# Kernel tuning notes

Hardware: AMD Instinct MI355X
Metric: run time of the kernel (lower is better)

## Reference

```python
import jax, jax.numpy as jnp
import numpy as np

HIDDEN = 512


def setup_inputs() -> dict:
    key = jax.random.key(0)
    ks = jax.random.split(key, 5)
    S, B, I, H = 256, 128, 1024, HIDDEN
    scale_ih = 1.0 / np.sqrt(H)
    return {
        "x": jax.random.normal(ks[0], (S, B, I), dtype=jnp.float32),
        "w_ih": jax.random.normal(ks[1], (4 * H, I), dtype=jnp.float32) * scale_ih,
        "w_hh": jax.random.normal(ks[2], (4 * H, H), dtype=jnp.float32) * scale_ih,
        "b_ih": jax.random.normal(ks[3], (4 * H,), dtype=jnp.float32) * scale_ih,
        "b_hh": jax.random.normal(ks[4], (4 * H,), dtype=jnp.float32) * scale_ih,
    }


def reference(x, w_ih, w_hh, b_ih, b_hh):
    # x: [S, B, I]. LSTMCell with PyTorch gate order (i, f, g, o).
    S, B, _ = x.shape
    H = HIDDEN
    bias = b_ih + b_hh  # fuse both biases

    def step(carry, xt):
        h, c = carry
        gates = xt @ w_ih.T + h @ w_hh.T + bias  # [B, 4H]
        i, f, g, o = jnp.split(gates, 4, axis=-1)
        i = jax.nn.sigmoid(i)
        f = jax.nn.sigmoid(f)
        g = jnp.tanh(g)
        o = jax.nn.sigmoid(o)
        c = f * c + i * g
        h = o * jnp.tanh(c)
        # original code's h[arange(B)] / c[arange(B)] is an identity gather: no-op
        return (h, c), None

    h0 = jnp.zeros((B, H), dtype=x.dtype)
    c0 = jnp.zeros((B, H), dtype=x.dtype)
    (h, c), _ = jax.lax.scan(step, (h0, c0), x)
    return h.sum()
```

## Files before the change

kernel.cpp:

```cpp
#include <hip/hip_runtime.h>

typedef __attribute__((ext_vector_type(8))) short short8;
typedef __attribute__((ext_vector_type(4))) float f32x4;

#define S_LEN 256
#define BATCH 128
#define IN_DIM 1024
#define HID 512
#define G4 2048

#define SENT 0xFFFFFFFFu

#define LSTM_BLOCKS 128
#define GEMM_WORKERS 128
#define TOT_BLOCKS (LSTM_BLOCKS + GEMM_WORKERS)
#define NT_PER_ROW 8
#define N_TILES (256 * NT_PER_ROW)

__device__ unsigned g_cnt[S_LEN];

__device__ __forceinline__ unsigned short f32_bf16(float f) {
  unsigned int u = __float_as_uint(f);
  u = (u + 0x7FFFu + ((u >> 16) & 1u)) >> 16;
  return (unsigned short)u;
}
__device__ __forceinline__ float bf16_f32(unsigned short h) {
  return __uint_as_float(((unsigned int)h) << 16);
}
__device__ __forceinline__ float sigm(float x) { return 1.0f / (1.0f + __expf(-x)); }
__device__ __forceinline__ float tanh_fast(float x) {
  return 1.0f - 2.0f / (__expf(2.0f * x) + 1.0f);
}
__device__ __forceinline__ unsigned ld_cnt(const unsigned* p) {
  return __hip_atomic_load(p, __ATOMIC_RELAXED, __HIP_MEMORY_SCOPE_AGENT);
}
__device__ __forceinline__ unsigned ld_u32_agent(const void* p) {
  return __hip_atomic_load((const unsigned*)p, __ATOMIC_RELAXED, __HIP_MEMORY_SCOPE_AGENT);
}

__device__ __forceinline__ void cvt4(const float* __restrict__ s,
                                     unsigned short* __restrict__ d, int i) {
  float4 v = *(const float4*)(s + (size_t)i * 4);
  ushort4 o;
  o.x = f32_bf16(v.x); o.y = f32_bf16(v.y); o.z = f32_bf16(v.z); o.w = f32_bf16(v.w);
  *(ushort4*)(d + (size_t)i * 4) = o;
}

__global__ void prep(const float* __restrict__ x, const float* __restrict__ w_ih,
                     const float* __restrict__ w_hh, const float* __restrict__ b_ih,
                     const float* __restrict__ b_hh, unsigned short* __restrict__ x_bf,
                     unsigned short* __restrict__ wih_bf, unsigned short* __restrict__ whh_bf,
                     float* __restrict__ bias, uint4* __restrict__ hring4) {
  const int gtid = blockIdx.x * blockDim.x + threadIdx.x;
  const int gsz = gridDim.x * blockDim.x;
  if (gtid < G4) bias[gtid] = b_ih[gtid] + b_hh[gtid];
  if (gtid < S_LEN) g_cnt[gtid] = 0u;
  for (int i = gtid; i < 33554432 / 4; i += gsz) cvt4(x, x_bf, i);
  for (int i = gtid; i < 2097152 / 4; i += gsz) cvt4(w_ih, wih_bf, i);
  for (int i = gtid; i < 1048576 / 4; i += gsz) cvt4(w_hh, whh_bf, i);
  const int SLOT4 = BATCH * HID / 8;
  const int TOT4 = 257 * SLOT4;
  const uint4 z = make_uint4(0u, 0u, 0u, 0u);
  const uint4 sN = make_uint4(SENT, SENT, SENT, SENT);
  for (int k = gtid; k < TOT4; k += gsz) hring4[k] = (k < SLOT4) ? z : sN;
}

__device__ __forceinline__ void gl_lds16(const void* g, void* l) {
  __builtin_amdgcn_global_load_lds(
      (const __attribute__((address_space(1))) unsigned int*)g,
      (__attribute__((address_space(3))) unsigned int*)l, 16, 0, 0);
}

__global__ __launch_bounds__(512, 1) void fused_lstm(
    const unsigned short* __restrict__ whh,
    const unsigned short* __restrict__ xbf,
    const unsigned short* __restrict__ wih,
    const float* __restrict__ bias,
    unsigned short* __restrict__ gx,
    unsigned* __restrict__ hring,
    float* __restrict__ out) {
  __shared__ __align__(16) union {
    struct { unsigned short Hs[2][16][520]; float Gt[16][132]; } L;
    struct { unsigned short As[2 * 4096]; unsigned short Bs[2 * 8192]; } G;
  } sm;

  const int tid = threadIdx.x;
  const int w = tid >> 6, l = tid & 63;

  if (blockIdx.x >= LSTM_BLOCKS) {
    const int wm = w & 1, wn = w >> 1;
    for (int tile = (int)blockIdx.x - LSTM_BLOCKS; tile < N_TILES; tile += GEMM_WORKERS) {
      const int nt = tile & (NT_PER_ROW - 1), mt = tile >> 3;
      f32x4 acc[4][4];
#pragma unroll
      for (int i = 0; i < 4; i++)
#pragma unroll
        for (int j = 0; j < 4; j++) acc[i][j] = f32x4{0.f, 0.f, 0.f, 0.f};

      auto stage = [&](int cur, int k0) {
        {
          int row = tid >> 2, kc = tid & 3;
          gl_lds16(xbf + (size_t)(mt * 128 + row) * 1024 + k0 + kc * 8,
                   sm.G.As + cur * 4096 + w * 512);
        }
#pragma unroll
        for (int jj = 0; jj < 2; ++jj) {
          int cid = jj * 512 + tid;
          int row = cid >> 2, kc = cid & 3;
          gl_lds16(wih + (size_t)(nt * 256 + row) * 1024 + k0 + kc * 8,
                   sm.G.Bs + cur * 8192 + jj * 4096 + w * 512);
        }
      };

      stage(0, 0);
      asm volatile("s_waitcnt vmcnt(0)" ::: "memory");
      __builtin_amdgcn_s_barrier();

      for (int ks = 0; ks < 32; ++ks) {
        const int cur = ks & 1;
        if (ks + 1 < 32) stage(cur ^ 1, (ks + 1) * 32);
        short8 a[4], b[4];
#pragma unroll
        for (int i = 0; i < 4; i++)
          a[i] = *(const short8*)&sm.G.As[cur * 4096 +
                                          (wm * 64 + i * 16 + (l & 15)) * 32 + (l >> 4) * 8];
#pragma unroll
        for (int j = 0; j < 4; j++)
          b[j] = *(const short8*)&sm.G.Bs[cur * 8192 +
                                          (wn * 64 + j * 16 + (l & 15)) * 32 + (l >> 4) * 8];
#pragma unroll
        for (int i = 0; i < 4; i++)
#pragma unroll
          for (int j = 0; j < 4; j++)
            acc[i][j] = __builtin_amdgcn_mfma_f32_16x16x32_bf16(a[i], b[j], acc[i][j], 0, 0, 0);
        __builtin_amdgcn_sched_barrier(0);
        asm volatile("s_waitcnt vmcnt(0)" ::: "memory");
        __builtin_amdgcn_s_barrier();
      }

#pragma unroll
      for (int j = 0; j < 4; j++) {
        int cg = nt * 256 + wn * 64 + j * 16 + (l & 15);
        float bv = bias[cg];
#pragma unroll
        for (int i = 0; i < 4; i++) {
          int rbase = mt * 128 + wm * 64 + i * 16 + (l >> 4) * 4;
#pragma unroll
          for (int r = 0; r < 4; r++) {
            unsigned short hv = f32_bf16(acc[i][j][r] + bv);
            __hip_atomic_store(gx + (size_t)(rbase + r) * G4 + cg, hv,
                               __ATOMIC_RELAXED, __HIP_MEMORY_SCOPE_AGENT);
          }
        }
      }
      asm volatile("s_waitcnt vmcnt(0)" ::: "memory");
      __syncthreads();
      if (tid == 0)
        __hip_atomic_fetch_add(&g_cnt[mt], 1u, __ATOMIC_RELAXED, __HIP_MEMORY_SCOPE_AGENT);
    }
    return;
  }

  __builtin_amdgcn_s_setprio(1);
  if (tid >= 256) {
    for (int t = 0; t < S_LEN; t++) __syncthreads();
    return;
  }
  const int m = blockIdx.x & 7;
  const int s = blockIdx.x >> 3;

  short8 bw[16][2];
#pragma unroll
  for (int u = 0; u < 2; u++) {
    int n = (2 * w + u) * 16 + (l & 15);
    int jn = n >> 2, g = n & 3;
    int R = g * 512 + s * 32 + jn;
    const unsigned short* base = whh + (size_t)R * 512 + ((l >> 4) * 8);
#pragma unroll
    for (int kk = 0; kk < 16; kk++) bw[kk][u] = *(const short8*)(base + kk * 32);
  }

  const int b = l & 15;
  const int p = 4 * w + (l >> 4);
  const int gb = m * 16 + b;
  const int colg = s * 32 + 2 * p;
  float c0 = 0.f, c1 = 0.f;
  unsigned hp_last = 0u;

  const int SLOTW = BATCH * HID / 2;
  const unsigned long long* hull = (const unsigned long long*)hring;
  const int SLOTQ = BATCH * HID / 4;

  const int skc = tid & 127;
  const int srow = tid >> 7;
  const bool selfst = (((tid >> 3) & 15) == s);
  const size_t qbase = (size_t)(m * 16 + srow) * 128 + skc;

  unsigned long long v[8];
#pragma unroll
  for (int it = 0; it < 8; it++)
    v[it] = __hip_atomic_load(&hull[qbase + (size_t)it * 256],
                              __ATOMIC_RELAXED, __HIP_MEMORY_SCOPE_AGENT);
  while (ld_cnt(&g_cnt[0]) != (unsigned)NT_PER_ROW) __builtin_amdgcn_s_sleep(2);
  float2 pg[4];
  {
    size_t base0 = (size_t)gb * G4 + colg;
#pragma unroll
    for (int g = 0; g < 4; g++) {
      unsigned u = ld_u32_agent(gx + base0 + (size_t)g * 512);
      pg[g].x = bf16_f32((unsigned short)(u & 0xFFFFu));
      pg[g].y = bf16_f32((unsigned short)(u >> 16));
    }
  }
  unsigned cn = ld_cnt(&g_cnt[1]);

  for (int t = 0; t < S_LEN; t++) {
    const int buf = t & 1;
    const unsigned long long* src = hull + (size_t)t * SLOTQ;

    if (!(selfst && t > 0)) {
      for (;;) {
        int bad = 0;
#pragma unroll
        for (int it = 0; it < 8; it++)
          bad |= (((unsigned)v[it] == SENT) | ((unsigned)(v[it] >> 32) == SENT)) << it;
        if (!bad) break;
#pragma unroll
        for (int it = 0; it < 8; it++)
          if ((bad >> it) & 1)
            v[it] = __hip_atomic_load(&src[qbase + (size_t)it * 256],
                                      __ATOMIC_RELAXED, __HIP_MEMORY_SCOPE_AGENT);
      }
#pragma unroll
      for (int it = 0; it < 8; it++)
        *(unsigned long long*)&sm.L.Hs[buf][it * 2 + srow][skc * 4] = v[it];
    }
    __syncthreads();

    unsigned long long vn[8];
    float2 pgn[4];
    if (t + 1 < S_LEN) {
      if (!selfst) {
        const unsigned long long* srcn = hull + (size_t)(t + 1) * SLOTQ;
#pragma unroll
        for (int it = 0; it < 8; it++)
          vn[it] = __hip_atomic_load(&srcn[qbase + (size_t)it * 256],
                                     __ATOMIC_RELAXED, __HIP_MEMORY_SCOPE_AGENT);
      }
      if (cn != (unsigned)NT_PER_ROW) {
        do {
          __builtin_amdgcn_s_sleep(1);
          cn = ld_cnt(&g_cnt[t + 1]);
        } while (cn != (unsigned)NT_PER_ROW);
      }
      size_t basen = (size_t)((t + 1) * BATCH + gb) * G4 + colg;
#pragma unroll
      for (int g = 0; g < 4; g++) {
        unsigned u = ld_u32_agent(gx + basen + (size_t)g * 512);
        pgn[g].x = bf16_f32((unsigned short)(u & 0xFFFFu));
        pgn[g].y = bf16_f32((unsigned short)(u >> 16));
      }
      cn = (t + 2 < S_LEN) ? ld_cnt(&g_cnt[t + 2]) : (unsigned)NT_PER_ROW;
    }

    f32x4 acc0 = f32x4{0.f, 0.f, 0.f, 0.f};
    f32x4 acc1 = f32x4{0.f, 0.f, 0.f, 0.f};
#pragma unroll
    for (int kk = 0; kk < 16; kk++) {
      short8 a = *(const short8*)&sm.L.Hs[buf][l & 15][kk * 32 + (l >> 4) * 8];
      acc0 = __builtin_amdgcn_mfma_f32_16x16x32_bf16(a, bw[kk][0], acc0, 0, 0, 0);
      acc1 = __builtin_amdgcn_mfma_f32_16x16x32_bf16(a, bw[kk][1], acc1, 0, 0, 0);
    }

#pragma unroll
    for (int r = 0; r < 4; r++) {
      sm.L.Gt[(l >> 4) * 4 + r][(2 * w + 0) * 16 + (l & 15)] = acc0[r];
      sm.L.Gt[(l >> 4) * 4 + r][(2 * w + 1) * 16 + (l & 15)] = acc1[r];
    }

    float4 g0 = *(const float4*)&sm.L.Gt[b][8 * p];
    float4 g1 = *(const float4*)&sm.L.Gt[b][8 * p + 4];
    float i0 = sigm(g0.x + pg[0].x), f0 = sigm(g0.y + pg[1].x);
    float gg0 = tanh_fast(g0.z + pg[2].x), o0 = sigm(g0.w + pg[3].x);
    c0 = f0 * c0 + i0 * gg0;
    float h0 = o0 * tanh_fast(c0);
    float i1 = sigm(g1.x + pg[0].y), f1 = sigm(g1.y + pg[1].y);
    float gg1 = tanh_fast(g1.z + pg[2].y), o1 = sigm(g1.w + pg[3].y);
    c1 = f1 * c1 + i1 * gg1;
    float h1 = o1 * tanh_fast(c1);
    unsigned hp = (unsigned)f32_bf16(h0) | ((unsigned)f32_bf16(h1) << 16);
    hp_last = hp;

    __hip_atomic_store(&hring[(size_t)(t + 1) * SLOTW + gb * 256 + s * 16 + p], hp,
                       __ATOMIC_RELAXED, __HIP_MEMORY_SCOPE_AGENT);
    *(unsigned*)&sm.L.Hs[buf ^ 1][b][colg] = hp;

#pragma unroll
    for (int it = 0; it < 8; it++) v[it] = vn[it];
#pragma unroll
    for (int g = 0; g < 4; g++) pg[g] = pgn[g];
  }

  {
    float loc = bf16_f32((unsigned short)(hp_last & 0xFFFFu)) +
                bf16_f32((unsigned short)(hp_last >> 16));
#pragma unroll
    for (int off = 32; off > 0; off >>= 1) loc += __shfl_down(loc, off);
    if (l == 0) atomicAdd(out, loc);
  }
}

extern "C" void kernel_launch(void* const* d_in, const int* in_sizes, int n_in,
                              void* d_out, int out_size, void* d_ws, size_t ws_size,
                              hipStream_t stream) {
  const float* x = (const float*)d_in[0];
  const float* w_ih = (const float*)d_in[1];
  const float* w_hh = (const float*)d_in[2];
  const float* b_ih = (const float*)d_in[3];
  const float* b_hh = (const float*)d_in[4];

  char* ws = (char*)d_ws;
  unsigned short* x_bf = (unsigned short*)(ws);
  unsigned short* wih_bf = (unsigned short*)(ws + 67108864);
  unsigned short* whh_bf = (unsigned short*)(ws + 71303168);
  float* bias = (float*)(ws + 73400320);
  unsigned* hring = (unsigned*)(ws + 73408512);
  unsigned short* gx = (unsigned short*)(ws + 107094016);

  prep<<<2048, 256, 0, stream>>>(x, w_ih, w_hh, b_ih, b_hh, x_bf, wih_bf, whh_bf, bias,
                                 (uint4*)hring);

  fused_lstm<<<TOT_BLOCKS, 512, 0, stream>>>(whh_bf, x_bf, wih_bf, bias, gx, hring,
                                             (float*)d_out);
}
```

Before: 1.080 ms.

## Fuse x fp32-to-bf16 conversion into GEMM worker A-tile staging

Drops the separate prep pass that converted the whole 128 MB fp32 x tensor to bf16. GEMM workers now load fp32 x rows into registers, convert them to bf16 and write them to LDS, overlapped with the MFMA loop. This removes a full write and re-read of x_bf before the fused kernel starts. The cost is twice the global read bytes for A inside the GEMM and extra conversion ALU work. It also adds an asm register pin on the resident W_hh fragments to keep them in VGPRs, and halves the prep grid.

```diff
diff --git a/kernel.cpp b/kernel.cpp
--- a/kernel.cpp
+++ b/kernel.cpp
@@ -2,6 +2,7 @@
 
 typedef __attribute__((ext_vector_type(8))) short short8;
 typedef __attribute__((ext_vector_type(4))) float f32x4;
+typedef __attribute__((ext_vector_type(4))) int i32x4;
 
 #define S_LEN 256
 #define BATCH 128
@@ -36,6 +37,11 @@
 }
 __device__ __forceinline__ unsigned ld_u32_agent(const void* p) {
   return __hip_atomic_load((const unsigned*)p, __ATOMIC_RELAXED, __HIP_MEMORY_SCOPE_AGENT);
+}
+__device__ __forceinline__ short8 pin8(short8 x) {
+  i32x4 t = __builtin_bit_cast(i32x4, x);
+  asm volatile("" : "+v"(t));
+  return __builtin_bit_cast(short8, t);
 }
 
 __device__ __forceinline__ void cvt4(const float* __restrict__ s,
@@ -46,16 +52,14 @@
   *(ushort4*)(d + (size_t)i * 4) = o;
 }
 
-__global__ void prep(const float* __restrict__ x, const float* __restrict__ w_ih,
-                     const float* __restrict__ w_hh, const float* __restrict__ b_ih,
-                     const float* __restrict__ b_hh, unsigned short* __restrict__ x_bf,
+__global__ void prep(const float* __restrict__ w_ih, const float* __restrict__ w_hh,
+                     const float* __restrict__ b_ih, const float* __restrict__ b_hh,
                      unsigned short* __restrict__ wih_bf, unsigned short* __restrict__ whh_bf,
                      float* __restrict__ bias, uint4* __restrict__ hring4) {
   const int gtid = blockIdx.x * blockDim.x + threadIdx.x;
   const int gsz = gridDim.x * blockDim.x;
   if (gtid < G4) bias[gtid] = b_ih[gtid] + b_hh[gtid];
   if (gtid < S_LEN) g_cnt[gtid] = 0u;
-  for (int i = gtid; i < 33554432 / 4; i += gsz) cvt4(x, x_bf, i);
   for (int i = gtid; i < 2097152 / 4; i += gsz) cvt4(w_ih, wih_bf, i);
   for (int i = gtid; i < 1048576 / 4; i += gsz) cvt4(w_hh, whh_bf, i);
   const int SLOT4 = BATCH * HID / 8;
@@ -73,7 +77,7 @@
 
 __global__ __launch_bounds__(512, 1) void fused_lstm(
     const unsigned short* __restrict__ whh,
-    const unsigned short* __restrict__ xbf,
+    const float* __restrict__ x,
     const unsigned short* __restrict__ wih,
     const float* __restrict__ bias,
     unsigned short* __restrict__ gx,
@@ -89,6 +93,7 @@
 
   if (blockIdx.x >= LSTM_BLOCKS) {
     const int wm = w & 1, wn = w >> 1;
+    const int arow = tid >> 2, akc = tid & 3;
     for (int tile = (int)blockIdx.x - LSTM_BLOCKS; tile < N_TILES; tile += GEMM_WORKERS) {
       const int nt = tile & (NT_PER_ROW - 1), mt = tile >> 3;
       f32x4 acc[4][4];
@@ -97,12 +102,9 @@
 #pragma unroll
         for (int j = 0; j < 4; j++) acc[i][j] = f32x4{0.f, 0.f, 0.f, 0.f};
 
-      auto stage = [&](int cur, int k0) {
-        {
-          int row = tid >> 2, kc = tid & 3;
-          gl_lds16(xbf + (size_t)(mt * 128 + row) * 1024 + k0 + kc * 8,
-                   sm.G.As + cur * 4096 + w * 512);
-        }
+      const float* xrow = x + (size_t)(mt * 128 + arow) * 1024 + akc * 8;
+
+      auto issueB = [&](int cur, int k0) {
 #pragma unroll
         for (int jj = 0; jj < 2; ++jj) {
           int cid = jj * 512 + tid;
@@ -111,14 +113,32 @@
                    sm.G.Bs + cur * 8192 + jj * 4096 + w * 512);
         }
       };
-
-      stage(0, 0);
-      asm volatile("s_waitcnt vmcnt(0)" ::: "memory");
+      auto issueX = [&](int k0, float4& xa, float4& xb) {
+        xa = *(const float4*)(xrow + k0);
+        xb = *(const float4*)(xrow + k0 + 4);
+      };
+      auto commitX = [&](int cur, const float4& xa, const float4& xb) {
+        uint4 o;
+        o.x = (unsigned)f32_bf16(xa.x) | ((unsigned)f32_bf16(xa.y) << 16);
+        o.y = (unsigned)f32_bf16(xa.z) | ((unsigned)f32_bf16(xa.w) << 16);
+        o.z = (unsigned)f32_bf16(xb.x) | ((unsigned)f32_bf16(xb.y) << 16);
+        o.w = (unsigned)f32_bf16(xb.z) | ((unsigned)f32_bf16(xb.w) << 16);
+        *(uint4*)&sm.G.As[cur * 4096 + tid * 8] = o;
+      };
+
+      float4 xa, xb;
+      issueX(0, xa, xb);
+      issueB(0, 0);
+      commitX(0, xa, xb);
+      asm volatile("s_waitcnt vmcnt(0) lgkmcnt(0)" ::: "memory");
       __builtin_amdgcn_s_barrier();
 
       for (int ks = 0; ks < 32; ++ks) {
         const int cur = ks & 1;
-        if (ks + 1 < 32) stage(cur ^ 1, (ks + 1) * 32);
+        if (ks + 1 < 32) {
+          issueX((ks + 1) * 32, xa, xb);
+          issueB(cur ^ 1, (ks + 1) * 32);
+        }
         short8 a[4], b[4];
 #pragma unroll
         for (int i = 0; i < 4; i++)
@@ -133,8 +153,9 @@
 #pragma unroll
           for (int j = 0; j < 4; j++)
             acc[i][j] = __builtin_amdgcn_mfma_f32_16x16x32_bf16(a[i], b[j], acc[i][j], 0, 0, 0);
+        if (ks + 1 < 32) commitX(cur ^ 1, xa, xb);
         __builtin_amdgcn_sched_barrier(0);
-        asm volatile("s_waitcnt vmcnt(0)" ::: "memory");
+        asm volatile("s_waitcnt vmcnt(0) lgkmcnt(0)" ::: "memory");
         __builtin_amdgcn_s_barrier();
       }
 
@@ -177,7 +198,7 @@
     int R = g * 512 + s * 32 + jn;
     const unsigned short* base = whh + (size_t)R * 512 + ((l >> 4) * 8);
 #pragma unroll
-    for (int kk = 0; kk < 16; kk++) bw[kk][u] = *(const short8*)(base + kk * 32);
+    for (int kk = 0; kk < 16; kk++) bw[kk][u] = pin8(*(const short8*)(base + kk * 32));
   }
 
   const int b = l & 15;
@@ -320,16 +341,15 @@
   const float* b_hh = (const float*)d_in[4];
 
   char* ws = (char*)d_ws;
-  unsigned short* x_bf = (unsigned short*)(ws);
   unsigned short* wih_bf = (unsigned short*)(ws + 67108864);
   unsigned short* whh_bf = (unsigned short*)(ws + 71303168);
   float* bias = (float*)(ws + 73400320);
   unsigned* hring = (unsigned*)(ws + 73408512);
   unsigned short* gx = (unsigned short*)(ws + 107094016);
 
-  prep<<<2048, 256, 0, stream>>>(x, w_ih, w_hh, b_ih, b_hh, x_bf, wih_bf, whh_bf, bias,
+  prep<<<1024, 256, 0, stream>>>(w_ih, w_hh, b_ih, b_hh, wih_bf, whh_bf, bias,
                                  (uint4*)hring);
 
-  fused_lstm<<<TOT_BLOCKS, 512, 0, stream>>>(whh_bf, x_bf, wih_bf, bias, gx, hring,
+  fused_lstm<<<TOT_BLOCKS, 512, 0, stream>>>(whh_bf, x, wih_bf, bias, gx, hring,
                                              (float*)d_out);
 }
```

Measured after the change: 1.107 ms. 1.03x slower.
